# Kernel tuning notes

Hardware: AMD Instinct MI355X
Metric: run time of the kernel (lower is better)

Reference implementation:

```python
import jax, jax.numpy as jnp
import numpy as np

HIDDEN = 2048
N_HEADS = 16
HEAD_DIM = HIDDEN // N_HEADS
SEQ = 4096
ROPE_BASE = 10000.0


def setup_inputs() -> dict:
    key = jax.random.key(0)
    ks = jax.random.split(key, 5)
    sc = 1.0 / np.sqrt(HIDDEN)
    return {
        "hidden_states": jax.random.normal(ks[0], (SEQ, HIDDEN), jnp.float32),
        "Wq": jax.random.normal(ks[1], (HIDDEN, HIDDEN), jnp.float32) * sc,
        "Wk": jax.random.normal(ks[2], (HIDDEN, HIDDEN), jnp.float32) * sc,
        "Wv": jax.random.normal(ks[3], (HIDDEN, HIDDEN), jnp.float32) * sc,
        "Wo": jax.random.normal(ks[4], (HIDDEN, HIDDEN), jnp.float32) * sc,
    }


def _rope_cos_sin(seq_len, head_dim, dtype):
    # Llama-style rotary embedding tables, shape [S, 1, head_dim]
    inv_freq = 1.0 / (ROPE_BASE ** (jnp.arange(0, head_dim, 2, dtype=jnp.float32) / head_dim))
    pos = jnp.arange(seq_len, dtype=jnp.float32)
    freqs = pos[:, None] * inv_freq[None, :]          # [S, d/2]
    emb = jnp.concatenate([freqs, freqs], axis=-1)     # [S, d]
    return jnp.cos(emb)[:, None, :].astype(dtype), jnp.sin(emb)[:, None, :].astype(dtype)


def _rotate_half(x):
    h = x.shape[-1] // 2
    return jnp.concatenate([-x[..., h:], x[..., :h]], axis=-1)


def reference(hidden_states, Wq, Wk, Wv, Wo):
    S, H = hidden_states.shape
    d = HEAD_DIM
    # QKV projections (nn.Linear: x @ W.T), split into heads: [S, nH, d]
    q = (hidden_states @ Wq.T).reshape(S, N_HEADS, d)
    k = (hidden_states @ Wk.T).reshape(S, N_HEADS, d)
    v = (hidden_states @ Wv.T).reshape(S, N_HEADS, d)
    # Per-position RoPE on q and k
    cos, sin = _rope_cos_sin(S, d, q.dtype)
    q = q * cos + _rotate_half(q) * sin
    k = k * cos + _rotate_half(k) * sin
    # Causal scaled-dot-product attention, scores [nH, S, S]
    scores = jnp.einsum("snd,tnd->nst", q, k) / jnp.sqrt(jnp.asarray(d, q.dtype))
    causal = jnp.tril(jnp.ones((S, S), dtype=bool))
    scores = jnp.where(causal[None, :, :], scores, jnp.asarray(-1e30, scores.dtype))
    probs = jax.nn.softmax(scores, axis=-1)
    ctx = jnp.einsum("nst,tnd->snd", probs, v).reshape(S, H)
    return ctx @ Wo.T
```

## Files before the change

kernel.cpp:

```cpp
#include <hip/hip_runtime.h>

#define SEQ 4096
#define HIDDEN 2048
#define NHEADS 16
#define HDIM 128
#define QBLK 128
#define WQ 32
#define KVB 64

typedef float f32x4 __attribute__((ext_vector_type(4)));
typedef __bf16 bf16x8 __attribute__((ext_vector_type(8)));
typedef unsigned int u32x4 __attribute__((ext_vector_type(4)));
typedef unsigned int u32x2 __attribute__((ext_vector_type(2)));
typedef unsigned short u16x8 __attribute__((ext_vector_type(8)));
typedef unsigned short u16x4 __attribute__((ext_vector_type(4)));
typedef unsigned short u16;

#define SCL2 0.12751747456918851f
#define RLOG 0.2076205059304601f

__device__ __forceinline__ u16 f2bf(float f) {
  unsigned u = __float_as_uint(f);
  unsigned r = 0x7fffu + ((u >> 16) & 1u);
  return (u16)((u + r) >> 16);
}
__device__ __forceinline__ float bf2f(u16 u) {
  return __uint_as_float(((unsigned)u) << 16);
}
__device__ __forceinline__ unsigned cvtpk(float a, float b) {
  unsigned r;
  asm volatile("v_cvt_pk_bf16_f32 %0, %1, %2" : "=v"(r) : "v"(a), "v"(b));
  return r;
}

__device__ __forceinline__ void gload16(const u16* g, u16* l) {
  __builtin_amdgcn_global_load_lds(
      (const __attribute__((address_space(1))) unsigned int*)g,
      (__attribute__((address_space(3))) unsigned int*)l, 16, 0, 0);
}

__device__ __forceinline__ int cumq(int q) {
  if (q < 16) return (q - 8) * 2;
  if (q < 24) return 16 + (q - 16) * 3;
  return 40 + (q - 24) * 4;
}

__global__ __launch_bounds__(256) void cvt5(const float* __restrict__ X,
    const float* __restrict__ Wq, const float* __restrict__ Wk,
    const float* __restrict__ Wv, const float* __restrict__ Wo,
    u16* __restrict__ dst) {
  const size_t SH = (size_t)SEQ * HIDDEN, HH = (size_t)HIDDEN * HIDDEN;
  size_t i = ((size_t)blockIdx.x * 256 + threadIdx.x) * 8;
  const float* src; size_t off;
  if (i < SH) { src = X; off = i; }
  else if (i < SH + HH) { src = Wq; off = i - SH; }
  else if (i < SH + 2 * HH) { src = Wk; off = i - SH - HH; }
  else if (i < SH + 3 * HH) { src = Wv; off = i - SH - 2 * HH; }
  else { src = Wo; off = i - SH - 3 * HH; }
  float4 a = *reinterpret_cast<const float4*>(src + off);
  float4 b = *reinterpret_cast<const float4*>(src + off + 4);
  u16x8 o;
  o[0] = f2bf(a.x); o[1] = f2bf(a.y); o[2] = f2bf(a.z); o[3] = f2bf(a.w);
  o[4] = f2bf(b.x); o[5] = f2bf(b.y); o[6] = f2bf(b.z); o[7] = f2bf(b.w);
  *reinterpret_cast<u32x4*>(dst + i) = __builtin_bit_cast(u32x4, o);
}

__global__ __launch_bounds__(256, 3) void gemm_qkv(const u16* __restrict__ Xb,
    const u16* __restrict__ Wqb, const u16* __restrict__ Wkb,
    const u16* __restrict__ Wvb, u16* __restrict__ Qo, u16* __restrict__ Ko,
    u16* __restrict__ Vt) {
  __shared__ u16 As[2][128 * 32];
  __shared__ u16 Bs[2][128 * 32];
  const int wg = blockIdx.x;
  const int swz = (wg & 7) * 192 + (wg >> 3);
  const int z = swz >> 9;
  const int rr_ = swz & 511;
  const u16 *A, *B;
  u16* C;
  int bm, bn, cst;
  if (z == 2) {
    A = Wvb; B = Xb; C = Vt;
    bm = (rr_ & 15) << 7; bn = (rr_ >> 4) << 7; cst = SEQ;
  } else {
    A = Xb; B = z ? Wkb : Wqb; C = z ? Ko : Qo;
    bm = (rr_ & 31) << 7; bn = (rr_ >> 5) << 7; cst = HIDDEN;
  }
  const int t = threadIdx.x, lane = t & 63, wave = t >> 6;
  const int lrow = lane & 15, lk = (lane >> 4) * 8;
  const int wr = wave * 32;
  const int r0 = t >> 2, c0 = (t & 3) * 8;

  f32x4 acc[2][8] = {};

#pragma unroll
  for (int is = 0; is < 2; ++is) {
    gload16(A + (size_t)(bm + is * 64 + r0) * HIDDEN + c0, &As[0][is * 2048 + t * 8]);
    gload16(B + (size_t)(bn + is * 64 + r0) * HIDDEN + c0, &Bs[0][is * 2048 + t * 8]);
  }
  __syncthreads();

  int p = 0;
  for (int kt = 0; kt < HIDDEN; kt += 32) {
    if (kt + 32 < HIDDEN) {
#pragma unroll
      for (int is = 0; is < 2; ++is) {
        gload16(A + (size_t)(bm + is * 64 + r0) * HIDDEN + kt + 32 + c0,
                &As[p ^ 1][is * 2048 + t * 8]);
        gload16(B + (size_t)(bn + is * 64 + r0) * HIDDEN + kt + 32 + c0,
                &Bs[p ^ 1][is * 2048 + t * 8]);
      }
    }
    bf16x8 af[2], bfv[8];
#pragma unroll
    for (int m = 0; m < 2; ++m)
      af[m] = __builtin_bit_cast(bf16x8,
          *reinterpret_cast<const u32x4*>(&As[p][(wr + m * 16 + lrow) * 32 + lk]));
#pragma unroll
    for (int n = 0; n < 8; ++n)
      bfv[n] = __builtin_bit_cast(bf16x8,
          *reinterpret_cast<const u32x4*>(&Bs[p][(n * 16 + lrow) * 32 + lk]));
#pragma unroll
    for (int n = 0; n < 8; ++n)
#pragma unroll
      for (int m = 0; m < 2; ++m)
        acc[m][n] = __builtin_amdgcn_mfma_f32_16x16x32_bf16(af[m], bfv[n], acc[m][n], 0, 0, 0);
    __syncthreads();
    p ^= 1;
  }

  const int rb = (lane >> 4) * 4;
  if (z < 2) {
#pragma unroll
    for (int m = 0; m < 2; ++m)
#pragma unroll
      for (int q = 0; q < 4; ++q) {
        const int s = bm + wr + m * 16 + rb + q;
#pragma unroll
        for (int n = 0; n < 4; ++n) {
          const int ii = n * 16 + lrow;
          float inv = exp2f((float)ii * -RLOG);
          float ang = (float)s * inv;
          float sn, cs;
          __sincosf(ang, &sn, &cs);
          float x1 = acc[m][n][q], x2 = acc[m][n + 4][q];
          acc[m][n][q] = x1 * cs - x2 * sn;
          acc[m][n + 4][q] = x2 * cs + x1 * sn;
        }
      }
  }
#pragma unroll
  for (int m = 0; m < 2; ++m)
#pragma unroll
    for (int n = 0; n < 8; ++n)
#pragma unroll
      for (int q = 0; q < 4; ++q)
        C[(size_t)(bm + wr + m * 16 + rb + q) * cst + bn + n * 16 + lrow] =
            f2bf(acc[m][n][q]);
}

__global__ __launch_bounds__(256, 3) void gemm_out(const u16* __restrict__ A,
    const u16* __restrict__ B, float* __restrict__ C) {
  __shared__ u16 As[2][128 * 32];
  __shared__ u16 Bs[2][128 * 32];
  const int wg = blockIdx.x;
  const int swz = (wg & 7) * 64 + (wg >> 3);
  const int bm = (swz & 31) << 7;
  const int bn = (swz >> 5) << 7;
  const int t = threadIdx.x, lane = t & 63, wave = t >> 6;
  const int lrow = lane & 15, lk = (lane >> 4) * 8;
  const int wr = wave * 32;
  const int r0 = t >> 2, c0 = (t & 3) * 8;

  f32x4 acc[2][8] = {};

#pragma unroll
  for (int is = 0; is < 2; ++is) {
    gload16(A + (size_t)(bm + is * 64 + r0) * HIDDEN + c0, &As[0][is * 2048 + t * 8]);
    gload16(B + (size_t)(bn + is * 64 + r0) * HIDDEN + c0, &Bs[0][is * 2048 + t * 8]);
  }
  __syncthreads();

  int p = 0;
  for (int kt = 0; kt < HIDDEN; kt += 32) {
    if (kt + 32 < HIDDEN) {
#pragma unroll
      for (int is = 0; is < 2; ++is) {
        gload16(A + (size_t)(bm + is * 64 + r0) * HIDDEN + kt + 32 + c0,
                &As[p ^ 1][is * 2048 + t * 8]);
        gload16(B + (size_t)(bn + is * 64 + r0) * HIDDEN + kt + 32 + c0,
                &Bs[p ^ 1][is * 2048 + t * 8]);
      }
    }
    bf16x8 af[2], bfv[8];
#pragma unroll
    for (int m = 0; m < 2; ++m)
      af[m] = __builtin_bit_cast(bf16x8,
          *reinterpret_cast<const u32x4*>(&As[p][(wr + m * 16 + lrow) * 32 + lk]));
#pragma unroll
    for (int n = 0; n < 8; ++n)
      bfv[n] = __builtin_bit_cast(bf16x8,
          *reinterpret_cast<const u32x4*>(&Bs[p][(n * 16 + lrow) * 32 + lk]));
#pragma unroll
    for (int n = 0; n < 8; ++n)
#pragma unroll
      for (int m = 0; m < 2; ++m)
        acc[m][n] = __builtin_amdgcn_mfma_f32_16x16x32_bf16(af[m], bfv[n], acc[m][n], 0, 0, 0);
    __syncthreads();
    p ^= 1;
  }

  const int rb = (lane >> 4) * 4;
#pragma unroll
  for (int m = 0; m < 2; ++m)
#pragma unroll
    for (int n = 0; n < 8; ++n)
#pragma unroll
      for (int q = 0; q < 4; ++q)
        C[(size_t)(bm + wr + m * 16 + rb + q) * HIDDEN + bn + n * 16 + lrow] =
            acc[m][n][q];
}

__global__ __launch_bounds__(256, 2) void attn_kernel(const u16* __restrict__ Q,
                                                      const u16* __restrict__ Kg,
                                                      const u16* __restrict__ Vt,
                                                      u16* __restrict__ O,
                                                      u16* __restrict__ Opart,
                                                      float* __restrict__ Ml) {
  __shared__ u16 Ks[2][KVB * 128];
  __shared__ u16 Vs[2][128 * KVB];
  __shared__ u16 Ps[4][WQ * KVB];
  const int t = threadIdx.x;
  const int wave = t >> 6;
  const int lane = t & 63;
  const int lrow = lane & 15;
  const int lgrp = lane >> 4;

  const int g = blockIdx.x;
  const int h = g / 80;
  const int e = 79 - (g - h * 80);
  int q, c, nc;
  if (e < 8)       { q = e;               c = 0;            nc = 1; }
  else if (e < 24) { q = 8 + ((e - 8) >> 1);  c = (e - 8) & 1;  nc = 2; }
  else if (e < 48) { q = 16 + (e - 24) / 3;   c = (e - 24) % 3; nc = 3; }
  else             { q = 24 + ((e - 48) >> 2); c = (e - 48) & 3; nc = 4; }
  const int total = 2 * q + 2;
  const int base = total / nc, rem = total - base * nc;
  const int it0 = c * base + (c < rem ? c : rem);
  const int it1 = it0 + base + (c < rem ? 1 : 0);

  const int qb0 = q * QBLK;
  const int qw = qb0 + wave * WQ;

  bf16x8 qf[2][4];
#pragma unroll
  for (int rowf = 0; rowf < 2; ++rowf)
#pragma unroll
    for (int kk = 0; kk < 4; ++kk)
      qf[rowf][kk] = __builtin_bit_cast(bf16x8, *reinterpret_cast<const u32x4*>(
          Q + (size_t)(qw + rowf * 16 + lrow) * HIDDEN + h * HDIM + kk * 32 + lgrp * 8));

  const u16* kgb[4]; const u16* vgb[4]; int kof[4], vof[4];
#pragma unroll
  for (int is = 0; is < 4; ++is) {
    int ch = is * 256 + t;
    int krow = ch >> 4, kslot = ch & 15;
    int kcol = ((kslot & 8) | ((kslot ^ krow) & 7)) * 8;
    kgb[is] = Kg + (size_t)krow * HIDDEN + h * HDIM + kcol;
    kof[is] = ch * 8;
    int vrow = ch >> 3, vslot = ch & 7;
    int vcol = ((vslot ^ vrow) & 7) * 8;
    vgb[is] = Vt + (size_t)(h * HDIM + vrow) * SEQ + vcol;
    vof[is] = ch * 8;
  }

  f32x4 acc[2][8] = {};
  float m2[2] = {-1e30f, -1e30f};
  float lsum[2] = {0.f, 0.f};

#pragma unroll
  for (int is = 0; is < 4; ++is) {
    gload16(kgb[is] + (size_t)(it0 * KVB) * HIDDEN, &Ks[0][kof[is]]);
    gload16(vgb[is] + it0 * KVB, &Vs[0][vof[is]]);
  }
  __syncthreads();

  int cur = 0;
  for (int bt = it0; bt < it1; ++bt) {
    const int t0 = bt * KVB;
    if (bt + 1 < it1) {
      const int t1 = (bt + 1) * KVB;
#pragma unroll
      for (int is = 0; is < 4; ++is) {
        gload16(kgb[is] + (size_t)t1 * HIDDEN, &Ks[cur ^ 1][kof[is]]);
        gload16(vgb[is] + t1, &Vs[cur ^ 1][vof[is]]);
      }
    }

    if (t0 <= qw + WQ - 1) {
      const bool need_mask = (t0 + KVB - 1 > qw);
      f32x4 sc[2][4] = {};
      __builtin_amdgcn_s_setprio(1);
#pragma unroll
      for (int kk = 0; kk < 4; ++kk) {
#pragma unroll
        for (int colf = 0; colf < 4; ++colf) {
          int trow = colf * 16 + lrow;
          int slot = kk * 4 + lgrp;
          bf16x8 kf = __builtin_bit_cast(bf16x8, *reinterpret_cast<const u32x4*>(
              &Ks[cur][trow * 128 + ((slot & 8) | ((slot ^ trow) & 7)) * 8]));
#pragma unroll
          for (int rowf = 0; rowf < 2; ++rowf)
            sc[rowf][colf] = __builtin_amdgcn_mfma_f32_16x16x32_bf16(
                kf, qf[rowf][kk], sc[rowf][colf], 0, 0, 0);
        }
      }
      __builtin_amdgcn_s_setprio(0);

      float pmax[2];
#pragma unroll
      for (int rowf = 0; rowf < 2; ++rowf) {
        const int qg = qw + rowf * 16 + lrow;
        float mx = -3.0e38f;
#pragma unroll
        for (int colf = 0; colf < 4; ++colf) {
          const int kvb0 = t0 + colf * 16 + lgrp * 4;
#pragma unroll
          for (int r = 0; r < 4; ++r) {
            float v = sc[rowf][colf][r] * SCL2;
            if (need_mask) v = (kvb0 + r <= qg) ? v : -1e30f;
            sc[rowf][colf][r] = v;
            mx = fmaxf(mx, v);
          }
        }
        mx = fmaxf(mx, __shfl_xor(mx, 16));
        mx = fmaxf(mx, __shfl_xor(mx, 32));
        pmax[rowf] = mx;
      }

      bool grow = (pmax[0] > m2[0] + 11.5f) || (pmax[1] > m2[1] + 11.5f);
      if (__any(grow)) {
#pragma unroll
        for (int rowf = 0; rowf < 2; ++rowf) {
          float mn = fmaxf(m2[rowf], pmax[rowf]);
          float sf = exp2f(m2[rowf] - mn);
          m2[rowf] = mn;
          lsum[rowf] *= sf;
#pragma unroll
          for (int r = 0; r < 4; ++r) {
            float sfr = __shfl(sf, (lane & 48) | (lgrp * 4 + r));
#pragma unroll
            for (int nn = 0; nn < 8; ++nn) acc[rowf][nn][r] *= sfr;
          }
        }
      }

#pragma unroll
      for (int rowf = 0; rowf < 2; ++rowf) {
        const int qq = rowf * 16 + lrow;
        float ps = 0.f;
#pragma unroll
        for (int colf = 0; colf < 4; ++colf) {
          float pv[4];
#pragma unroll
          for (int r = 0; r < 4; ++r) {
            pv[r] = exp2f(sc[rowf][colf][r] - m2[rowf]);
            ps += pv[r];
          }
          u32x2 pk2;
          pk2[0] = cvtpk(pv[0], pv[1]);
          pk2[1] = cvtpk(pv[2], pv[3]);
          const int kv = colf * 16 + lgrp * 4;
          const int sw = (kv >> 3) ^ (qq & 7);
          *reinterpret_cast<u32x2*>(&Ps[wave][qq * 64 + sw * 8 + (kv & 7)]) = pk2;
        }
        ps += __shfl_xor(ps, 16);
        ps += __shfl_xor(ps, 32);
        lsum[rowf] += ps;
      }

      __builtin_amdgcn_s_setprio(1);
#pragma unroll
      for (int ks = 0; ks < 2; ++ks) {
        bf16x8 pa[2];
#pragma unroll
        for (int rowf = 0; rowf < 2; ++rowf) {
          const int qq = rowf * 16 + lrow;
          const int sl = ks * 4 + lgrp;
          pa[rowf] = __builtin_bit_cast(bf16x8, *reinterpret_cast<const u32x4*>(
              &Ps[wave][qq * 64 + (sl ^ (qq & 7)) * 8]));
        }
#pragma unroll
        for (int nn = 0; nn < 8; ++nn) {
          const int d = nn * 16 + lrow;
          bf16x8 vb = __builtin_bit_cast(bf16x8, *reinterpret_cast<const u32x4*>(
              &Vs[cur][d * 64 + (((ks * 4 + lgrp) ^ d) & 7) * 8]));
#pragma unroll
          for (int rowf = 0; rowf < 2; ++rowf)
            acc[rowf][nn] = __builtin_amdgcn_mfma_f32_16x16x32_bf16(
                pa[rowf], vb, acc[rowf][nn], 0, 0, 0);
        }
      }
      __builtin_amdgcn_s_setprio(0);
    }

    __syncthreads();
    cur ^= 1;
  }

  if (nc == 1) {
#pragma unroll
    for (int rowf = 0; rowf < 2; ++rowf) {
      float inv[4];
#pragma unroll
      for (int r = 0; r < 4; ++r) {
        float lsr = __shfl(lsum[rowf], (lane & 48) | (lgrp * 4 + r));
        inv[r] = 1.0f / lsr;
      }
#pragma unroll
      for (int nn = 0; nn < 8; ++nn)
#pragma unroll
        for (int r = 0; r < 4; ++r) {
          int row = qw + rowf * 16 + lgrp * 4 + r;
          int col = h * HDIM + nn * 16 + lrow;
          O[(size_t)row * HIDDEN + col] = f2bf(acc[rowf][nn][r] * inv[r]);
        }
    }
  } else {
    const int slot = h * 72 + cumq(q) + c;
    u16* Op = Opart + (size_t)slot * (QBLK * HDIM);
    float* ml = Ml + (size_t)slot * 256;
#pragma unroll
    for (int rowf = 0; rowf < 2; ++rowf) {
#pragma unroll
      for (int nn = 0; nn < 8; ++nn)
#pragma unroll
        for (int r = 0; r < 4; ++r) {
          int rl = wave * 32 + rowf * 16 + lgrp * 4 + r;
          Op[rl * HDIM + nn * 16 + lrow] = f2bf(acc[rowf][nn][r]);
        }
      if (lgrp == 0) {
        int rl = wave * 32 + rowf * 16 + lrow;
        ml[rl] = m2[rowf];
        ml[128 + rl] = lsum[rowf];
      }
    }
  }
}

__global__ __launch_bounds__(256) void combine_kernel(const u16* __restrict__ Opart,
                                                      const float* __restrict__ Ml,
                                                      u16* __restrict__ O) {
  const int bid = blockIdx.x;
  const int h = bid / 24;
  const int q = 8 + bid % 24;
  const int nc = q / 8 + 1;
  const int sbase = h * 72 + cumq(q);
  const int r = threadIdx.x >> 1;
  const int d0 = (threadIdx.x & 1) * 64;

  float w[4], l = 0.f, M = -3.0e38f;
#pragma unroll
  for (int c = 0; c < 4; ++c)
    if (c < nc) M = fmaxf(M, Ml[(size_t)(sbase + c) * 256 + r]);
#pragma unroll
  for (int c = 0; c < 4; ++c)
    if (c < nc) {
      w[c] = exp2f(Ml[(size_t)(sbase + c) * 256 + r] - M);
      l += w[c] * Ml[(size_t)(sbase + c) * 256 + 128 + r];
    }
  const float inv = 1.0f / l;

  for (int dd = 0; dd < 64; dd += 8) {
    float a8[8] = {};
#pragma unroll
    for (int c = 0; c < 4; ++c)
      if (c < nc) {
        u16x8 v = *reinterpret_cast<const u16x8*>(
            Opart + (size_t)(sbase + c) * (QBLK * HDIM) + r * HDIM + d0 + dd);
#pragma unroll
        for (int j = 0; j < 8; ++j) a8[j] += w[c] * bf2f(v[j]);
      }
    u16x8 o8;
#pragma unroll
    for (int j = 0; j < 8; ++j) o8[j] = f2bf(a8[j] * inv);
    *reinterpret_cast<u16x8*>(
        &O[(size_t)(q * QBLK + r) * HIDDEN + h * HDIM + d0 + dd]) = o8;
  }
}

extern "C" void kernel_launch(void* const* d_in, const int* in_sizes, int n_in,
                              void* d_out, int out_size, void* d_ws, size_t ws_size,
                              hipStream_t stream) {
  const float* X  = (const float*)d_in[0];
  const float* Wq = (const float*)d_in[1];
  const float* Wk = (const float*)d_in[2];
  const float* Wv = (const float*)d_in[3];
  const float* Wo = (const float*)d_in[4];
  float* out = (float*)d_out;

  u16* ws = (u16*)d_ws;
  const size_t SH = (size_t)SEQ * HIDDEN;
  const size_t HH = (size_t)HIDDEN * HIDDEN;
  u16* Xb  = ws;
  u16* Wqb = Xb + SH;
  u16* Wkb = Wqb + HH;
  u16* Wvb = Wkb + HH;
  u16* Wob = Wvb + HH;
  u16* Qb  = Wob + HH;
  u16* Kb  = Qb + SH;
  u16* Vtb = Kb + SH;
  u16* Cb  = Vtb + SH;

  u16* Opart = ws;
  float* Ml = (float*)(ws + (size_t)1152 * 16384);

  cvt5<<<(int)((SH + 4 * HH) / 2048), 256, 0, stream>>>(X, Wq, Wk, Wv, Wo, ws);

  gemm_qkv<<<1536, 256, 0, stream>>>(Xb, Wqb, Wkb, Wvb, Qb, Kb, Vtb);

  attn_kernel<<<1280, 256, 0, stream>>>(Qb, Kb, Vtb, Cb, Opart, Ml);
  combine_kernel<<<384, 256, 0, stream>>>(Opart, Ml, Cb);

  gemm_out<<<512, 256, 0, stream>>>(Cb, Wob, out);
}
```

Measured before the change: 384.1 us.

## Keep P in registers, single-buffer K, fold softmax scale into Q, rebalance attention split

The attention kernel no longer stages the softmax probabilities through shared memory. It reuses the QK^T accumulator layout directly as the PV A-operand, which is possible because V's output columns are permuted in the QKV GEMM epilogue. The K tile becomes single-buffered with a mid-iteration barrier, and the Ps buffer is dropped, cutting LDS enough for 3 blocks per CU. The softmax scale is folded into the Q RoPE epilogue, and the KV split schedule changes to at most 3 chunks with 960 blocks and a smaller combine grid. The risks are less overlap of the K load, an extra barrier per iteration, and more register pressure at the higher occupancy target.

```diff
diff --git a/kernel.cpp b/kernel.cpp
--- a/kernel.cpp
+++ b/kernel.cpp
@@ -13,7 +13,6 @@
 typedef unsigned int u32x4 __attribute__((ext_vector_type(4)));
 typedef unsigned int u32x2 __attribute__((ext_vector_type(2)));
 typedef unsigned short u16x8 __attribute__((ext_vector_type(8)));
-typedef unsigned short u16x4 __attribute__((ext_vector_type(4)));
 typedef unsigned short u16;
 
 #define SCL2 0.12751747456918851f
@@ -40,9 +39,7 @@
 }
 
 __device__ __forceinline__ int cumq(int q) {
-  if (q < 16) return (q - 8) * 2;
-  if (q < 24) return 16 + (q - 16) * 3;
-  return 40 + (q - 24) * 4;
+  return q < 24 ? (q - 12) * 2 : 24 + (q - 24) * 3;
 }
 
 __global__ __launch_bounds__(256) void cvt5(const float* __restrict__ X,
@@ -130,6 +127,7 @@
 
   const int rb = (lane >> 4) * 4;
   if (z < 2) {
+    const float qscale = (z == 0) ? SCL2 : 1.0f;
 #pragma unroll
     for (int m = 0; m < 2; ++m)
 #pragma unroll
@@ -142,6 +140,7 @@
           float ang = (float)s * inv;
           float sn, cs;
           __sincosf(ang, &sn, &cs);
+          sn *= qscale; cs *= qscale;
           float x1 = acc[m][n][q], x2 = acc[m][n + 4][q];
           acc[m][n][q] = x1 * cs - x2 * sn;
           acc[m][n + 4][q] = x2 * cs + x1 * sn;
@@ -153,9 +152,15 @@
 #pragma unroll
     for (int n = 0; n < 8; ++n)
 #pragma unroll
-      for (int q = 0; q < 4; ++q)
-        C[(size_t)(bm + wr + m * 16 + rb + q) * cst + bn + n * 16 + lrow] =
-            f2bf(acc[m][n][q]);
+      for (int q = 0; q < 4; ++q) {
+        int col;
+        if (z == 2)
+          col = bn + (n >> 2) * 64 + ((n >> 1) & 1) * 32 + (lrow >> 2) * 8 +
+                (n & 1) * 4 + (lrow & 3);
+        else
+          col = bn + n * 16 + lrow;
+        C[(size_t)(bm + wr + m * 16 + rb + q) * cst + col] = f2bf(acc[m][n][q]);
+      }
 }
 
 __global__ __launch_bounds__(256, 3) void gemm_out(const u16* __restrict__ A,
@@ -220,15 +225,14 @@
             acc[m][n][q];
 }
 
-__global__ __launch_bounds__(256, 2) void attn_kernel(const u16* __restrict__ Q,
+__global__ __launch_bounds__(256, 3) void attn_kernel(const u16* __restrict__ Q,
                                                       const u16* __restrict__ Kg,
                                                       const u16* __restrict__ Vt,
                                                       u16* __restrict__ O,
                                                       u16* __restrict__ Opart,
                                                       float* __restrict__ Ml) {
-  __shared__ u16 Ks[2][KVB * 128];
+  __shared__ u16 Ks[KVB * 128];
   __shared__ u16 Vs[2][128 * KVB];
-  __shared__ u16 Ps[4][WQ * KVB];
   const int t = threadIdx.x;
   const int wave = t >> 6;
   const int lane = t & 63;
@@ -236,20 +240,18 @@
   const int lgrp = lane >> 4;
 
   const int g = blockIdx.x;
-  const int h = g / 80;
-  const int e = 79 - (g - h * 80);
+  const int h = g & 15;
+  const int e = g >> 4;
   int q, c, nc;
-  if (e < 8)       { q = e;               c = 0;            nc = 1; }
-  else if (e < 24) { q = 8 + ((e - 8) >> 1);  c = (e - 8) & 1;  nc = 2; }
-  else if (e < 48) { q = 16 + (e - 24) / 3;   c = (e - 24) % 3; nc = 3; }
-  else             { q = 24 + ((e - 48) >> 2); c = (e - 48) & 3; nc = 4; }
+  if (e < 24)      { q = 24 + e / 3;           c = e % 3;         nc = 3; }
+  else if (e < 48) { q = 23 - ((e - 24) >> 1); c = (e - 24) & 1;  nc = 2; }
+  else             { q = 59 - e;               c = 0;             nc = 1; }
   const int total = 2 * q + 2;
   const int base = total / nc, rem = total - base * nc;
   const int it0 = c * base + (c < rem ? c : rem);
   const int it1 = it0 + base + (c < rem ? 1 : 0);
 
-  const int qb0 = q * QBLK;
-  const int qw = qb0 + wave * WQ;
+  const int qw = q * QBLK + wave * WQ;
 
   bf16x8 qf[2][4];
 #pragma unroll
@@ -279,26 +281,17 @@
 
 #pragma unroll
   for (int is = 0; is < 4; ++is) {
-    gload16(kgb[is] + (size_t)(it0 * KVB) * HIDDEN, &Ks[0][kof[is]]);
+    gload16(kgb[is] + (size_t)(it0 * KVB) * HIDDEN, &Ks[kof[is]]);
     gload16(vgb[is] + it0 * KVB, &Vs[0][vof[is]]);
   }
   __syncthreads();
 
-  int cur = 0;
+  int p = 0;
   for (int bt = it0; bt < it1; ++bt) {
     const int t0 = bt * KVB;
-    if (bt + 1 < it1) {
-      const int t1 = (bt + 1) * KVB;
-#pragma unroll
-      for (int is = 0; is < 4; ++is) {
-        gload16(kgb[is] + (size_t)t1 * HIDDEN, &Ks[cur ^ 1][kof[is]]);
-        gload16(vgb[is] + t1, &Vs[cur ^ 1][vof[is]]);
-      }
-    }
-
-    if (t0 <= qw + WQ - 1) {
-      const bool need_mask = (t0 + KVB - 1 > qw);
-      f32x4 sc[2][4] = {};
+    const bool live = (t0 <= qw + WQ - 1);
+    f32x4 sc[2][4] = {};
+    if (live) {
       __builtin_amdgcn_s_setprio(1);
 #pragma unroll
       for (int kk = 0; kk < 4; ++kk) {
@@ -307,7 +300,7 @@
           int trow = colf * 16 + lrow;
           int slot = kk * 4 + lgrp;
           bf16x8 kf = __builtin_bit_cast(bf16x8, *reinterpret_cast<const u32x4*>(
-              &Ks[cur][trow * 128 + ((slot & 8) | ((slot ^ trow) & 7)) * 8]));
+              &Ks[trow * 128 + ((slot & 8) | ((slot ^ trow) & 7)) * 8]));
 #pragma unroll
           for (int rowf = 0; rowf < 2; ++rowf)
             sc[rowf][colf] = __builtin_amdgcn_mfma_f32_16x16x32_bf16(
@@ -315,7 +308,21 @@
         }
       }
       __builtin_amdgcn_s_setprio(0);
-
+    }
+
+    __syncthreads();
+
+    if (bt + 1 < it1) {
+      const int t1 = (bt + 1) * KVB;
+#pragma unroll
+      for (int is = 0; is < 4; ++is) {
+        gload16(kgb[is] + (size_t)t1 * HIDDEN, &Ks[kof[is]]);
+        gload16(vgb[is] + t1, &Vs[p ^ 1][vof[is]]);
+      }
+    }
+
+    if (live) {
+      const bool need_mask = (t0 + KVB - 1 > qw);
       float pmax[2];
 #pragma unroll
       for (int rowf = 0; rowf < 2; ++rowf) {
@@ -326,7 +333,7 @@
           const int kvb0 = t0 + colf * 16 + lgrp * 4;
 #pragma unroll
           for (int r = 0; r < 4; ++r) {
-            float v = sc[rowf][colf][r] * SCL2;
+            float v = sc[rowf][colf][r];
             if (need_mask) v = (kvb0 + r <= qg) ? v : -1e30f;
             sc[rowf][colf][r] = v;
             mx = fmaxf(mx, v);
@@ -354,9 +361,9 @@
         }
       }
 
+      unsigned paw[2][2][4];
 #pragma unroll
       for (int rowf = 0; rowf < 2; ++rowf) {
-        const int qq = rowf * 16 + lrow;
         float ps = 0.f;
 #pragma unroll
         for (int colf = 0; colf < 4; ++colf) {
@@ -366,12 +373,8 @@
             pv[r] = exp2f(sc[rowf][colf][r] - m2[rowf]);
             ps += pv[r];
           }
-          u32x2 pk2;
-          pk2[0] = cvtpk(pv[0], pv[1]);
-          pk2[1] = cvtpk(pv[2], pv[3]);
-          const int kv = colf * 16 + lgrp * 4;
-          const int sw = (kv >> 3) ^ (qq & 7);
-          *reinterpret_cast<u32x2*>(&Ps[wave][qq * 64 + sw * 8 + (kv & 7)]) = pk2;
+          paw[rowf][colf >> 1][(colf & 1) * 2 + 0] = cvtpk(pv[0], pv[1]);
+          paw[rowf][colf >> 1][(colf & 1) * 2 + 1] = cvtpk(pv[2], pv[3]);
         }
         ps += __shfl_xor(ps, 16);
         ps += __shfl_xor(ps, 32);
@@ -384,16 +387,15 @@
         bf16x8 pa[2];
 #pragma unroll
         for (int rowf = 0; rowf < 2; ++rowf) {
-          const int qq = rowf * 16 + lrow;
-          const int sl = ks * 4 + lgrp;
-          pa[rowf] = __builtin_bit_cast(bf16x8, *reinterpret_cast<const u32x4*>(
-              &Ps[wave][qq * 64 + (sl ^ (qq & 7)) * 8]));
+          u32x4 w = {paw[rowf][ks][0], paw[rowf][ks][1],
+                     paw[rowf][ks][2], paw[rowf][ks][3]};
+          pa[rowf] = __builtin_bit_cast(bf16x8, w);
         }
 #pragma unroll
         for (int nn = 0; nn < 8; ++nn) {
           const int d = nn * 16 + lrow;
           bf16x8 vb = __builtin_bit_cast(bf16x8, *reinterpret_cast<const u32x4*>(
-              &Vs[cur][d * 64 + (((ks * 4 + lgrp) ^ d) & 7) * 8]));
+              &Vs[p][d * 64 + (((ks * 4 + lgrp) ^ d) & 7) * 8]));
 #pragma unroll
           for (int rowf = 0; rowf < 2; ++rowf)
             acc[rowf][nn] = __builtin_amdgcn_mfma_f32_16x16x32_bf16(
@@ -404,7 +406,7 @@
     }
 
     __syncthreads();
-    cur ^= 1;
+    p ^= 1;
   }
 
   if (nc == 1) {
@@ -426,7 +428,7 @@
         }
     }
   } else {
-    const int slot = h * 72 + cumq(q) + c;
+    const int slot = h * 48 + cumq(q) + c;
     u16* Op = Opart + (size_t)slot * (QBLK * HDIM);
     float* ml = Ml + (size_t)slot * 256;
 #pragma unroll
@@ -451,19 +453,19 @@
                                                       const float* __restrict__ Ml,
                                                       u16* __restrict__ O) {
   const int bid = blockIdx.x;
-  const int h = bid / 24;
-  const int q = 8 + bid % 24;
-  const int nc = q / 8 + 1;
-  const int sbase = h * 72 + cumq(q);
+  const int h = bid / 20;
+  const int q = 12 + bid % 20;
+  const int nc = (q < 24) ? 2 : 3;
+  const int sbase = h * 48 + cumq(q);
   const int r = threadIdx.x >> 1;
   const int d0 = (threadIdx.x & 1) * 64;
 
-  float w[4], l = 0.f, M = -3.0e38f;
-#pragma unroll
-  for (int c = 0; c < 4; ++c)
+  float w[3], l = 0.f, M = -3.0e38f;
+#pragma unroll
+  for (int c = 0; c < 3; ++c)
     if (c < nc) M = fmaxf(M, Ml[(size_t)(sbase + c) * 256 + r]);
 #pragma unroll
-  for (int c = 0; c < 4; ++c)
+  for (int c = 0; c < 3; ++c)
     if (c < nc) {
       w[c] = exp2f(Ml[(size_t)(sbase + c) * 256 + r] - M);
       l += w[c] * Ml[(size_t)(sbase + c) * 256 + 128 + r];
@@ -473,7 +475,7 @@
   for (int dd = 0; dd < 64; dd += 8) {
     float a8[8] = {};
 #pragma unroll
-    for (int c = 0; c < 4; ++c)
+    for (int c = 0; c < 3; ++c)
       if (c < nc) {
         u16x8 v = *reinterpret_cast<const u16x8*>(
             Opart + (size_t)(sbase + c) * (QBLK * HDIM) + r * HDIM + d0 + dd);
@@ -512,14 +514,14 @@
   u16* Cb  = Vtb + SH;
 
   u16* Opart = ws;
-  float* Ml = (float*)(ws + (size_t)1152 * 16384);
+  float* Ml = (float*)(ws + (size_t)768 * 16384);
 
   cvt5<<<(int)((SH + 4 * HH) / 2048), 256, 0, stream>>>(X, Wq, Wk, Wv, Wo, ws);
 
   gemm_qkv<<<1536, 256, 0, stream>>>(Xb, Wqb, Wkb, Wvb, Qb, Kb, Vtb);
 
-  attn_kernel<<<1280, 256, 0, stream>>>(Qb, Kb, Vtb, Cb, Opart, Ml);
-  combine_kernel<<<384, 256, 0, stream>>>(Opart, Ml, Cb);
+  attn_kernel<<<960, 256, 0, stream>>>(Qb, Kb, Vtb, Cb, Opart, Ml);
+  combine_kernel<<<320, 256, 0, stream>>>(Opart, Ml, Cb);
 
   gemm_out<<<512, 256, 0, stream>>>(Cb, Wob, out);
 }
```

Result: slower. 470.9 us (+22.6%).
